# Optimization experiments

Measured on AMD Instinct MI355X. Metric: run time of the kernel, lower is better.

Reference implementation:

```python
import jax, jax.numpy as jnp
import numpy as np

HIDDEN = 1024
HEADS = 16
HEAD_DIM = HIDDEN // HEADS


def setup_inputs() -> dict:
    key = jax.random.key(0)
    k1, k2, k3, k4, k5 = jax.random.split(key, 5)
    scale = 1.0 / np.sqrt(HIDDEN)
    return {
        "query": jax.random.normal(k1, (8, 1024, HIDDEN), dtype=jnp.float32),
        "w_qkv": jax.random.normal(k2, (HIDDEN, 3 * HIDDEN), dtype=jnp.float32) * scale,
        "b_qkv": jnp.zeros((3 * HIDDEN,), dtype=jnp.float32),
        "w_o": jax.random.normal(k3, (HIDDEN, HIDDEN), dtype=jnp.float32) * scale,
        "b_o": jnp.zeros((HIDDEN,), dtype=jnp.float32),
    }


def reference(query, w_qkv, b_qkv, w_o, b_o):
    B, S, _ = query.shape
    qkv = query @ w_qkv + b_qkv                      # [B,S,3H]
    q, k, v = jnp.split(qkv, 3, axis=-1)
    # split heads -> [B, heads, S, head_dim]
    def sh(x):
        return x.reshape(B, S, HEADS, HEAD_DIM).transpose(0, 2, 1, 3)
    qh, kh, vh = sh(q), sh(k), sh(v)
    qh = qh * (HEAD_DIM ** -0.5)
    logits = jnp.einsum("bhqd,bhkd->bhqk", qh, kh)   # [B,H,S,S]
    weights = jax.nn.softmax(logits, axis=-1)        # dropout p=0.0 -> identity
    x = jnp.einsum("bhqk,bhkd->bhqd", weights, vh)
    x = x.transpose(0, 2, 1, 3).reshape(B, S, HIDDEN)
    return x @ w_o + b_o
```

## Files before the change

kernel.cpp:

```cpp
#include <hip/hip_runtime.h>
#include <math.h>

#define BATCH   8
#define SEQ     1024
#define HIDDEN  1024
#define NHEADS  16
#define HDIM    64
#define MROWS   (BATCH * SEQ)

typedef __bf16 bf16x8 __attribute__((ext_vector_type(8)));
typedef float  f32x4  __attribute__((ext_vector_type(4)));

__device__ __forceinline__ unsigned short f2bf(float f) {
    union { float f; unsigned int u; } v; v.f = f;
    unsigned int u = v.u;
    u += 0x7fffu + ((u >> 16) & 1u);
    return (unsigned short)(u >> 16);
}

__device__ __forceinline__ unsigned int pack2bf_trunc(float a, float b) {
    union { float f; unsigned int u; } ua, ub;
    ua.f = a; ub.f = b;
    return (ua.u >> 16) | (ub.u & 0xFFFF0000u);
}

__device__ __forceinline__ void gl2lds16(const unsigned short* g, unsigned short* l) {
    __builtin_amdgcn_global_load_lds(
        (const __attribute__((address_space(1))) void*)g,
        (__attribute__((address_space(3))) void*)l, 16, 0, 0);
}

__global__ __launch_bounds__(256) void prep_kernel(
    const float* __restrict__ query, unsigned short* __restrict__ queryBf,
    const float* __restrict__ wqkv,  unsigned short* __restrict__ wqkvT,
    const float* __restrict__ wo,    unsigned short* __restrict__ woT) {
    __shared__ float tile[32][33];
    const int bid = blockIdx.x;
    const int tid = threadIdx.x;

    if (bid < 8192) {
        int i = bid * 256 + tid;
        float4 v = reinterpret_cast<const float4*>(query)[i];
        ushort4 o;
        o.x = f2bf(v.x); o.y = f2bf(v.y); o.z = f2bf(v.z); o.w = f2bf(v.w);
        reinterpret_cast<ushort4*>(queryBf)[i] = o;
        return;
    }

    const float* in;
    unsigned short* out;
    int R, C, bx, by;
    if (bid < 8192 + 3072) {
        int b = bid - 8192;
        in = wqkv; out = wqkvT; R = HIDDEN; C = 3 * HIDDEN;
        bx = b % 96; by = b / 96;
    } else {
        int b = bid - 11264;
        in = wo; out = woT; R = HIDDEN; C = HIDDEN;
        bx = b % 32; by = b / 32;
    }
    const int tx = tid & 31, ty = tid >> 5;
    const int x  = bx * 32 + tx;
    const int y0 = by * 32;
#pragma unroll
    for (int j = 0; j < 32; j += 8)
        tile[ty + j][tx] = in[(size_t)(y0 + ty + j) * C + x];
    __syncthreads();
    const int x2 = y0 + tx;
    const int y2 = bx * 32;
#pragma unroll
    for (int j = 0; j < 32; j += 8)
        out[(size_t)(y2 + ty + j) * R + x2] = f2bf(tile[tx][ty + j]);
}

template <int EPI>
__global__ __launch_bounds__(256) void gemm_bt_kernel(
    const unsigned short* __restrict__ A,
    const unsigned short* __restrict__ Bt,
    const float* __restrict__ bias,
    unsigned short* __restrict__ out_bf,
    float* __restrict__ out_f,
    int M, int N, int K) {
    __shared__ __align__(16) unsigned short As[128 * 64];
    __shared__ __align__(16) unsigned short Bs[128 * 64];

    const int tid  = threadIdx.x;
    const int wid  = tid >> 6;
    const int lane = tid & 63;
    const int l15  = lane & 15;
    const int quad = lane >> 4;
    const int wm   = (wid & 1) * 64;
    const int wn   = (wid >> 1) * 64;

    const int npn = N >> 7;
    const int pid = blockIdx.x;
    const int ppg = 4 * npn;
    const int gid = pid / ppg;
    const int loc = pid - gid * ppg;
    const int pm  = gid * 4 + (loc & 3);
    const int pn  = loc >> 2;
    const int m0  = pm * 128;
    const int n0  = pn * 128;

    const int srow = wid * 32 + (lane >> 3);
    const int skcs = ((lane & 7) ^ (lane >> 3)) * 8;
    const int rsw  = lane & 7;

    f32x4 acc[4][4];
#pragma unroll
    for (int i = 0; i < 4; ++i)
#pragma unroll
        for (int j = 0; j < 4; ++j) acc[i][j] = (f32x4){0.f, 0.f, 0.f, 0.f};

    for (int kt = 0; kt < K; kt += 64) {
        __syncthreads();
#pragma unroll
        for (int it = 0; it < 4; ++it) {
            int row = srow + it * 8;
            gl2lds16(A  + (size_t)(m0 + row) * K + kt + skcs, As + (wid * 32 + it * 8) * 64);
            gl2lds16(Bt + (size_t)(n0 + row) * K + kt + skcs, Bs + (wid * 32 + it * 8) * 64);
        }
        __syncthreads();
#pragma unroll
        for (int ks = 0; ks < 2; ++ks) {
            bf16x8 afr[4], bfr[4];
#pragma unroll
            for (int i = 0; i < 4; ++i)
                afr[i] = *reinterpret_cast<const bf16x8*>(
                    As + (wm + i * 16 + l15) * 64 + ((ks * 4 + quad) ^ rsw) * 8);
#pragma unroll
            for (int j = 0; j < 4; ++j)
                bfr[j] = *reinterpret_cast<const bf16x8*>(
                    Bs + (wn + j * 16 + l15) * 64 + ((ks * 4 + quad) ^ rsw) * 8);
#pragma unroll
            for (int i = 0; i < 4; ++i)
#pragma unroll
                for (int j = 0; j < 4; ++j)
                    acc[i][j] = __builtin_amdgcn_mfma_f32_16x16x32_bf16(afr[i], bfr[j], acc[i][j], 0, 0, 0);
        }
    }

#pragma unroll
    for (int j = 0; j < 4; ++j) {
        int col   = n0 + wn + j * 16 + l15;
        float bv  = bias[col];
        if constexpr (EPI == 0) {
            int which = col >> 10;
            int rem   = col & 1023;
            int h     = rem >> 6, d = rem & 63;
            if (which == 2) {
#pragma unroll
                for (int i = 0; i < 4; ++i) {
                    int row0 = m0 + wm + i * 16 + quad * 4;
                    int b    = row0 >> 10, s0 = row0 & 1023;
                    ushort4 o;
                    o.x = f2bf(acc[i][j][0] + bv);
                    o.y = f2bf(acc[i][j][1] + bv);
                    o.z = f2bf(acc[i][j][2] + bv);
                    o.w = f2bf(acc[i][j][3] + bv);
                    size_t idx = ((size_t)(2 * BATCH * NHEADS) +
                                  (size_t)b * NHEADS + h) * (SEQ * HDIM) +
                                 (size_t)d * SEQ + s0;
                    *reinterpret_cast<ushort4*>(out_bf + idx) = o;
                }
            } else {
                float sc = (which == 0) ? 0.18033688011112042f : 1.0f;
#pragma unroll
                for (int i = 0; i < 4; ++i)
#pragma unroll
                    for (int r = 0; r < 4; ++r) {
                        int row = m0 + wm + i * 16 + quad * 4 + r;
                        int b   = row >> 10, s = row & 1023;
                        float v = (acc[i][j][r] + bv) * sc;
                        size_t idx = ((((size_t)which * BATCH + b) * NHEADS + h) * SEQ + s) * HDIM + d;
                        out_bf[idx] = f2bf(v);
                    }
            }
        } else {
#pragma unroll
            for (int i = 0; i < 4; ++i)
#pragma unroll
                for (int r = 0; r < 4; ++r) {
                    int row = m0 + wm + i * 16 + quad * 4 + r;
                    out_f[(size_t)row * N + col] = acc[i][j][r] + bv;
                }
        }
    }
}

__global__ __launch_bounds__(256) void gemm_bt64_kernel(
    const unsigned short* __restrict__ A,
    const unsigned short* __restrict__ Bt,
    const float* __restrict__ bias,
    float* __restrict__ out_f,
    int M, int N, int K) {
    __shared__ __align__(16) unsigned short As[64 * 64];
    __shared__ __align__(16) unsigned short Bs[128 * 64];

    const int tid  = threadIdx.x;
    const int wid  = tid >> 6;
    const int lane = tid & 63;
    const int l15  = lane & 15;
    const int quad = lane >> 4;
    const int wm   = (wid & 1) * 32;
    const int wn   = (wid >> 1) * 64;

    const int npn = N >> 7;
    const int pid = blockIdx.x;
    const int ppg = 4 * npn;
    const int gid = pid / ppg;
    const int loc = pid - gid * ppg;
    const int pm  = gid * 4 + (loc & 3);
    const int pn  = loc >> 2;
    const int m0  = pm * 64;
    const int n0  = pn * 128;

    const int srow = wid * 8 + (lane >> 3);
    const int skcs = ((lane & 7) ^ (lane >> 3)) * 8;
    const int rsw  = lane & 7;

    f32x4 acc[2][4];
#pragma unroll
    for (int i = 0; i < 2; ++i)
#pragma unroll
        for (int j = 0; j < 4; ++j) acc[i][j] = (f32x4){0.f, 0.f, 0.f, 0.f};

    for (int kt = 0; kt < K; kt += 64) {
        __syncthreads();
#pragma unroll
        for (int it = 0; it < 2; ++it) {
            int row = srow + it * 32;
            gl2lds16(A + (size_t)(m0 + row) * K + kt + skcs,
                     As + (wid * 8 + it * 32) * 64);
        }
#pragma unroll
        for (int it = 0; it < 4; ++it) {
            int row = srow + it * 32;
            gl2lds16(Bt + (size_t)(n0 + row) * K + kt + skcs,
                     Bs + (wid * 8 + it * 32) * 64);
        }
        __syncthreads();
#pragma unroll
        for (int ks = 0; ks < 2; ++ks) {
            bf16x8 afr[2], bfr[4];
#pragma unroll
            for (int i = 0; i < 2; ++i)
                afr[i] = *reinterpret_cast<const bf16x8*>(
                    As + (wm + i * 16 + l15) * 64 + ((ks * 4 + quad) ^ rsw) * 8);
#pragma unroll
            for (int j = 0; j < 4; ++j)
                bfr[j] = *reinterpret_cast<const bf16x8*>(
                    Bs + (wn + j * 16 + l15) * 64 + ((ks * 4 + quad) ^ rsw) * 8);
#pragma unroll
            for (int i = 0; i < 2; ++i)
#pragma unroll
                for (int j = 0; j < 4; ++j)
                    acc[i][j] = __builtin_amdgcn_mfma_f32_16x16x32_bf16(afr[i], bfr[j], acc[i][j], 0, 0, 0);
        }
    }

#pragma unroll
    for (int j = 0; j < 4; ++j) {
        int col   = n0 + wn + j * 16 + l15;
        float bv  = bias[col];
#pragma unroll
        for (int i = 0; i < 2; ++i)
#pragma unroll
            for (int r = 0; r < 4; ++r) {
                int row = m0 + wm + i * 16 + quad * 4 + r;
                out_f[(size_t)row * N + col] = acc[i][j][r] + bv;
            }
    }
}

__global__ __launch_bounds__(256, 3) void attn_kernel(
    const unsigned short* __restrict__ qkv,
    const unsigned short* __restrict__ vt,
    unsigned short* __restrict__ x) {
    constexpr int LDP = 68;
    __shared__ __align__(16) unsigned short Ks[2][64 * 64];
    __shared__ __align__(16) unsigned short Vs[2][64 * 64];
    __shared__ __align__(16) unsigned short PQ[4][32 * LDP];

    unsigned short* Qs = &PQ[0][0];

    const int tid  = threadIdx.x;
    const int wid  = tid >> 6;
    const int lane = tid & 63;
    const int l15  = lane & 15;
    const int quad = lane >> 4;
    const int srow8 = lane >> 3;
    const int skcs  = ((lane & 7) ^ srow8) * 8;
    const int rsw   = lane & 7;

    const int id = blockIdx.x;
    const int bh = (id & 7) * 16 + (id >> 6);
    const int q0 = ((id >> 3) & 7) * 128;

    const unsigned short* Qg  = qkv + (size_t)bh * SEQ * HDIM;
    const unsigned short* Kg  = qkv + (size_t)(128 + bh) * SEQ * HDIM;
    const unsigned short* VTg = vt + (size_t)bh * SEQ * HDIM;

    auto stageKV = [&](int t0s, int buf) {
#pragma unroll
        for (int it = 0; it < 2; ++it) {
            int row = wid * 16 + it * 8 + srow8;
            int sK = ((lane & 7) ^ (wid * 2 + it)) * 8;
            gl2lds16(Kg + (size_t)(t0s + row) * HDIM + sK,
                     Ks[buf] + (wid * 16 + it * 8) * 64);
            gl2lds16(VTg + (size_t)row * SEQ + t0s + skcs,
                     Vs[buf] + (wid * 16 + it * 8) * 64);
        }
    };

#pragma unroll
    for (int it = 0; it < 4; ++it) {
        gl2lds16(Qg + (size_t)(q0 + wid * 32 + it * 8 + srow8) * HDIM + skcs,
                 Qs + (wid * 32 + it * 8) * 64);
    }
    stageKV(0, 0);
    __syncthreads();

    bf16x8 qf[2][2];
#pragma unroll
    for (int m = 0; m < 2; ++m)
#pragma unroll
        for (int h = 0; h < 2; ++h)
            qf[m][h] = *reinterpret_cast<const bf16x8*>(
                Qs + (wid * 32 + m * 16 + l15) * 64 + ((h * 4 + quad) ^ rsw) * 8);
    __syncthreads();

    float lsum[2][4];
    f32x4 accO[2][4];
#pragma unroll
    for (int m = 0; m < 2; ++m)
#pragma unroll
        for (int r = 0; r < 4; ++r) lsum[m][r] = 0.f;
#pragma unroll
    for (int m = 0; m < 2; ++m)
#pragma unroll
        for (int jd = 0; jd < 4; ++jd) accO[m][jd] = (f32x4){0.f, 0.f, 0.f, 0.f};

    for (int t0 = 0; t0 < SEQ; t0 += 64) {
        const int cur = (t0 >> 6) & 1;
        if (t0 + 64 < SEQ) stageKV(t0 + 64, cur ^ 1);

        f32x4 accL[2][4];
#pragma unroll
        for (int m = 0; m < 2; ++m)
#pragma unroll
            for (int j = 0; j < 4; ++j) accL[m][j] = (f32x4){0.f, 0.f, 0.f, 0.f};
#pragma unroll
        for (int j = 0; j < 4; ++j) {
            int krow = l15 * 4 + j;
            int kru  = krow >> 3;
            bf16x8 kf0 = *reinterpret_cast<const bf16x8*>(
                Ks[cur] + krow * 64 + ((0 + quad) ^ kru) * 8);
            bf16x8 kf1 = *reinterpret_cast<const bf16x8*>(
                Ks[cur] + krow * 64 + ((4 + quad) ^ kru) * 8);
#pragma unroll
            for (int m = 0; m < 2; ++m) {
                accL[m][j] = __builtin_amdgcn_mfma_f32_16x16x32_bf16(qf[m][0], kf0, accL[m][j], 0, 0, 0);
                accL[m][j] = __builtin_amdgcn_mfma_f32_16x16x32_bf16(qf[m][1], kf1, accL[m][j], 0, 0, 0);
            }
        }

#pragma unroll
        for (int m = 0; m < 2; ++m)
#pragma unroll
            for (int r = 0; r < 4; ++r) {
                float p0 = __builtin_amdgcn_exp2f(accL[m][0][r]);
                float p1 = __builtin_amdgcn_exp2f(accL[m][1][r]);
                float p2 = __builtin_amdgcn_exp2f(accL[m][2][r]);
                float p3 = __builtin_amdgcn_exp2f(accL[m][3][r]);
                lsum[m][r] += (p0 + p1) + (p2 + p3);
                uint2 pk;
                pk.x = pack2bf_trunc(p0, p1);
                pk.y = pack2bf_trunc(p2, p3);
                *reinterpret_cast<uint2*>(
                    &PQ[wid][(m * 16 + quad * 4 + r) * LDP + l15 * 4]) = pk;
            }

        bf16x8 pf[2][2];
#pragma unroll
        for (int m = 0; m < 2; ++m)
#pragma unroll
            for (int h = 0; h < 2; ++h)
                pf[m][h] = *reinterpret_cast<const bf16x8*>(
                    PQ[wid] + (m * 16 + l15) * LDP + h * 32 + quad * 8);
#pragma unroll
        for (int jd = 0; jd < 4; ++jd) {
            bf16x8 vf0 = *reinterpret_cast<const bf16x8*>(
                Vs[cur] + (jd * 16 + l15) * 64 + ((0 + quad) ^ rsw) * 8);
            bf16x8 vf1 = *reinterpret_cast<const bf16x8*>(
                Vs[cur] + (jd * 16 + l15) * 64 + ((4 + quad) ^ rsw) * 8);
#pragma unroll
            for (int m = 0; m < 2; ++m) {
                accO[m][jd] = __builtin_amdgcn_mfma_f32_16x16x32_bf16(pf[m][0], vf0, accO[m][jd], 0, 0, 0);
                accO[m][jd] = __builtin_amdgcn_mfma_f32_16x16x32_bf16(pf[m][1], vf1, accO[m][jd], 0, 0, 0);
            }
        }

        __syncthreads();
    }

    const int b = bh >> 4, h = bh & 15;
#pragma unroll
    for (int m = 0; m < 2; ++m)
#pragma unroll
        for (int r = 0; r < 4; ++r) {
            float s = lsum[m][r];
            s += __shfl_xor(s, 1);
            s += __shfl_xor(s, 2);
            s += __shfl_xor(s, 4);
            s += __shfl_xor(s, 8);
            float inv = 1.0f / s;
            int srow = q0 + wid * 32 + m * 16 + quad * 4 + r;
            size_t base = ((size_t)b * SEQ + srow) * HIDDEN + h * HDIM;
#pragma unroll
            for (int jd = 0; jd < 4; ++jd)
                x[base + jd * 16 + l15] = f2bf(accO[m][jd][r] * inv);
        }
}

extern "C" void kernel_launch(void* const* d_in, const int* in_sizes, int n_in,
                              void* d_out, int out_size, void* d_ws, size_t ws_size,
                              hipStream_t stream) {
    const float* query = (const float*)d_in[0];
    const float* w_qkv = (const float*)d_in[1];
    const float* b_qkv = (const float*)d_in[2];
    const float* w_o   = (const float*)d_in[3];
    const float* b_o   = (const float*)d_in[4];
    float* out = (float*)d_out;

    unsigned short* ws = (unsigned short*)d_ws;
    unsigned short* queryBf = ws;
    unsigned short* wqkvT   = queryBf + (size_t)MROWS * HIDDEN;
    unsigned short* woT     = wqkvT + (size_t)3 * HIDDEN * HIDDEN;
    unsigned short* qkvbuf  = woT + (size_t)HIDDEN * HIDDEN;
    unsigned short* xbuf    = qkvbuf + (size_t)3 * MROWS * HIDDEN;
    unsigned short* vtbuf   = qkvbuf + (size_t)2 * BATCH * NHEADS * SEQ * HDIM;

    prep_kernel<<<dim3(12288), 256, 0, stream>>>(
        query, queryBf, w_qkv, wqkvT, w_o, woT);

    gemm_bt_kernel<0><<<dim3((MROWS / 128) * (3 * HIDDEN / 128)), 256, 0, stream>>>(
        queryBf, wqkvT, b_qkv, qkvbuf, nullptr, MROWS, 3 * HIDDEN, HIDDEN);

    attn_kernel<<<dim3(1024), 256, 0, stream>>>(qkvbuf, vtbuf, xbuf);

    gemm_bt64_kernel<<<dim3((MROWS / 64) * (HIDDEN / 128)), 256, 0, stream>>>(
        xbuf, woT, b_o, out, MROWS, HIDDEN, HIDDEN);
}
```

Measured before the change: 242.7 us.

## Enlarge output-projection GEMM tiles and double attention block query rows

The output-projection GEMM moves from 64x128 tiles with a K-step of 64 to 128x128 tiles with a K-step of 128. The LDS swizzle is widened to 16 chunks to match. The attention kernel now runs 512 threads per block and covers 256 query rows, halving the grid, so each staged K/V tile is reused by twice as many query rows. The aims are to reduce global-memory traffic per FLOP and to cut block count and staging overhead. The risks are higher register and LDS use per block, fewer blocks in flight, and a tail-effect change on the smaller grids.

```diff
diff --git a/kernel.cpp b/kernel.cpp
--- a/kernel.cpp
+++ b/kernel.cpp
@@ -188,21 +188,21 @@
     }
 }
 
-__global__ __launch_bounds__(256) void gemm_bt64_kernel(
+__global__ __launch_bounds__(256) void gemm_bt_k128_kernel(
     const unsigned short* __restrict__ A,
     const unsigned short* __restrict__ Bt,
     const float* __restrict__ bias,
     float* __restrict__ out_f,
     int M, int N, int K) {
-    __shared__ __align__(16) unsigned short As[64 * 64];
-    __shared__ __align__(16) unsigned short Bs[128 * 64];
+    __shared__ __align__(16) unsigned short As[128 * 128];
+    __shared__ __align__(16) unsigned short Bs[128 * 128];
 
     const int tid  = threadIdx.x;
     const int wid  = tid >> 6;
     const int lane = tid & 63;
     const int l15  = lane & 15;
     const int quad = lane >> 4;
-    const int wm   = (wid & 1) * 32;
+    const int wm   = (wid & 1) * 64;
     const int wn   = (wid >> 1) * 64;
 
     const int npn = N >> 7;
@@ -212,47 +212,42 @@
     const int loc = pid - gid * ppg;
     const int pm  = gid * 4 + (loc & 3);
     const int pn  = loc >> 2;
-    const int m0  = pm * 64;
+    const int m0  = pm * 128;
     const int n0  = pn * 128;
 
-    const int srow = wid * 8 + (lane >> 3);
-    const int skcs = ((lane & 7) ^ (lane >> 3)) * 8;
-    const int rsw  = lane & 7;
-
-    f32x4 acc[2][4];
-#pragma unroll
-    for (int i = 0; i < 2; ++i)
+    const int srow4 = wid * 4 + (lane >> 4);
+    const int skc   = ((lane & 15) ^ (srow4 & 15)) * 8;
+
+    f32x4 acc[4][4];
+#pragma unroll
+    for (int i = 0; i < 4; ++i)
 #pragma unroll
         for (int j = 0; j < 4; ++j) acc[i][j] = (f32x4){0.f, 0.f, 0.f, 0.f};
 
-    for (int kt = 0; kt < K; kt += 64) {
+    for (int kt = 0; kt < K; kt += 128) {
         __syncthreads();
 #pragma unroll
-        for (int it = 0; it < 2; ++it) {
-            int row = srow + it * 32;
-            gl2lds16(A + (size_t)(m0 + row) * K + kt + skcs,
-                     As + (wid * 8 + it * 32) * 64);
-        }
-#pragma unroll
-        for (int it = 0; it < 4; ++it) {
-            int row = srow + it * 32;
-            gl2lds16(Bt + (size_t)(n0 + row) * K + kt + skcs,
-                     Bs + (wid * 8 + it * 32) * 64);
+        for (int it = 0; it < 8; ++it) {
+            int row = srow4 + it * 16;
+            gl2lds16(A  + (size_t)(m0 + row) * K + kt + skc,
+                     As + (it * 16 + wid * 4) * 128);
+            gl2lds16(Bt + (size_t)(n0 + row) * K + kt + skc,
+                     Bs + (it * 16 + wid * 4) * 128);
         }
         __syncthreads();
 #pragma unroll
-        for (int ks = 0; ks < 2; ++ks) {
-            bf16x8 afr[2], bfr[4];
-#pragma unroll
-            for (int i = 0; i < 2; ++i)
+        for (int ks = 0; ks < 4; ++ks) {
+            bf16x8 afr[4], bfr[4];
+#pragma unroll
+            for (int i = 0; i < 4; ++i)
                 afr[i] = *reinterpret_cast<const bf16x8*>(
-                    As + (wm + i * 16 + l15) * 64 + ((ks * 4 + quad) ^ rsw) * 8);
+                    As + (wm + i * 16 + l15) * 128 + ((ks * 4 + quad) ^ l15) * 8);
 #pragma unroll
             for (int j = 0; j < 4; ++j)
                 bfr[j] = *reinterpret_cast<const bf16x8*>(
-                    Bs + (wn + j * 16 + l15) * 64 + ((ks * 4 + quad) ^ rsw) * 8);
-#pragma unroll
-            for (int i = 0; i < 2; ++i)
+                    Bs + (wn + j * 16 + l15) * 128 + ((ks * 4 + quad) ^ l15) * 8);
+#pragma unroll
+            for (int i = 0; i < 4; ++i)
 #pragma unroll
                 for (int j = 0; j < 4; ++j)
                     acc[i][j] = __builtin_amdgcn_mfma_f32_16x16x32_bf16(afr[i], bfr[j], acc[i][j], 0, 0, 0);
@@ -264,7 +259,7 @@
         int col   = n0 + wn + j * 16 + l15;
         float bv  = bias[col];
 #pragma unroll
-        for (int i = 0; i < 2; ++i)
+        for (int i = 0; i < 4; ++i)
 #pragma unroll
             for (int r = 0; r < 4; ++r) {
                 int row = m0 + wm + i * 16 + quad * 4 + r;
@@ -273,14 +268,14 @@
     }
 }
 
-__global__ __launch_bounds__(256, 3) void attn_kernel(
+__global__ __launch_bounds__(512, 4) void attn_kernel(
     const unsigned short* __restrict__ qkv,
     const unsigned short* __restrict__ vt,
     unsigned short* __restrict__ x) {
     constexpr int LDP = 68;
     __shared__ __align__(16) unsigned short Ks[2][64 * 64];
     __shared__ __align__(16) unsigned short Vs[2][64 * 64];
-    __shared__ __align__(16) unsigned short PQ[4][32 * LDP];
+    __shared__ __align__(16) unsigned short PQ[8][32 * LDP];
 
     unsigned short* Qs = &PQ[0][0];
 
@@ -294,23 +289,18 @@
     const int rsw   = lane & 7;
 
     const int id = blockIdx.x;
-    const int bh = (id & 7) * 16 + (id >> 6);
-    const int q0 = ((id >> 3) & 7) * 128;
+    const int bh = (id & 7) * 16 + (id >> 5);
+    const int q0 = ((id >> 3) & 3) * 256;
 
     const unsigned short* Qg  = qkv + (size_t)bh * SEQ * HDIM;
     const unsigned short* Kg  = qkv + (size_t)(128 + bh) * SEQ * HDIM;
     const unsigned short* VTg = vt + (size_t)bh * SEQ * HDIM;
 
     auto stageKV = [&](int t0s, int buf) {
-#pragma unroll
-        for (int it = 0; it < 2; ++it) {
-            int row = wid * 16 + it * 8 + srow8;
-            int sK = ((lane & 7) ^ (wid * 2 + it)) * 8;
-            gl2lds16(Kg + (size_t)(t0s + row) * HDIM + sK,
-                     Ks[buf] + (wid * 16 + it * 8) * 64);
-            gl2lds16(VTg + (size_t)row * SEQ + t0s + skcs,
-                     Vs[buf] + (wid * 16 + it * 8) * 64);
-        }
+        int row = wid * 8 + srow8;
+        int sK  = ((lane & 7) ^ wid) * 8;
+        gl2lds16(Kg + (size_t)(t0s + row) * HDIM + sK, Ks[buf] + wid * 8 * 64);
+        gl2lds16(VTg + (size_t)row * SEQ + t0s + skcs, Vs[buf] + wid * 8 * 64);
     };
 
 #pragma unroll
@@ -447,8 +437,8 @@
     gemm_bt_kernel<0><<<dim3((MROWS / 128) * (3 * HIDDEN / 128)), 256, 0, stream>>>(
         queryBf, wqkvT, b_qkv, qkvbuf, nullptr, MROWS, 3 * HIDDEN, HIDDEN);
 
-    attn_kernel<<<dim3(1024), 256, 0, stream>>>(qkvbuf, vtbuf, xbuf);
-
-    gemm_bt64_kernel<<<dim3((MROWS / 64) * (HIDDEN / 128)), 256, 0, stream>>>(
+    attn_kernel<<<dim3(512), 512, 0, stream>>>(qkvbuf, vtbuf, xbuf);
+
+    gemm_bt_k128_kernel<<<dim3((MROWS / 128) * (HIDDEN / 128)), 256, 0, stream>>>(
         xbuf, woT, b_o, out, MROWS, HIDDEN, HIDDEN);
 }
```

Result: faster. 225.9 us (-6.9%).
